# Performance work log

Hardware: AMD Instinct MI355X
Metric: run time of the kernel (lower is better)

Reference implementation:

```python
import jax, jax.numpy as jnp
import numpy as np
from jax import lax

T, B, R = 128, 128, 512  # timesteps, batch_size, read_size


def setup_inputs() -> dict:
    key = jax.random.key(0)
    ks = jax.random.split(key, 5)
    return {
        "u":  jax.random.uniform(ks[0], (T, B, 1), dtype=jnp.float32),
        "d1": jax.random.uniform(ks[1], (T, B, 1), dtype=jnp.float32),
        "d2": jax.random.uniform(ks[2], (T, B, 1), dtype=jnp.float32),
        "v1": jax.random.normal(ks[3], (T, B, R), dtype=jnp.float32),
        "v2": jax.random.normal(ks[4], (T, B, R), dtype=jnp.float32),
    }


def _forward(u, d1, d2, v1, v2):
    # Stack-style neural memory: each step pushes two (strength, value) slots,
    # reads up to total strength u from the top of the stack, then pops strength u.
    Tn, Bn, _ = u.shape
    Rn = v1.shape[-1]
    nslots = 2 * Tn
    # Pre-allocated slot store; unused slots have S=0, V=0 and contribute exactly 0
    # to both the read summary and strength_used, matching the growing-list semantics.
    S0 = jnp.zeros((nslots, Bn, 1), dtype=u.dtype)
    V0 = jnp.zeros((nslots, Bn, Rn), dtype=v1.dtype)

    def step(carry, inp):
        S, V = carry
        u_t, d1_t, d2_t, v1_t, v2_t, t = inp
        # push(d1, d2, v1, v2)
        S = S.at[2 * t].set(d1_t).at[2 * t + 1].set(d2_t)
        V = V.at[2 * t].set(v1_t).at[2 * t + 1].set(v2_t)
        Srev = S[::-1]  # stack order: top (most recent) first
        Vrev = V[::-1]

        # read(u): sequential scan over slots with strength bookkeeping
        def read_step(c, sv):
            summary, used = c
            s_i, v_i = sv
            # NOTE: torch.max(u - strength_used) is a GLOBAL max over the (B,1)
            # tensor (0-dim scalar), faithfully reproduced here.
            scal = jnp.max(u_t - used)
            summary = summary + v_i * jnp.minimum(s_i, scal)
            return (summary, used + s_i), None

        (summary, _), _ = lax.scan(
            read_step,
            (jnp.zeros((Bn, Rn), u.dtype), jnp.zeros((Bn, 1), u.dtype)),
            (Srev, Vrev),
        )

        # pop(u): elementwise strength depletion, same slot order
        def pop_step(used, s_i):
            s_new = s_i - jnp.minimum(s_i, jnp.maximum(jnp.zeros_like(s_i), u_t - used))
            return used + s_i, s_new

        _, Srev_new = lax.scan(pop_step, jnp.zeros((Bn, 1), u.dtype), Srev)
        return (Srev_new[::-1], V), summary

    xs = (u, d1, d2, v1, v2, jnp.arange(Tn))
    (_, _), outs = lax.scan(step, (S0, V0), xs)
    return outs  # (T, B, R) read contents per step


def reference(u, d1, d2, v1, v2):
    return _forward(u, d1, d2, v1, v2)
```

## Files before the change

### kernel.cpp

```cpp
#include <hip/hip_runtime.h>
#include <hip/hip_bf16.h>
#include <math.h>

constexpr int T = 128;
constexpr int B = 128;
constexpr int R = 512;
constexpr int NS = 256;

typedef __attribute__((ext_vector_type(8))) short bf16x8;
typedef __attribute__((ext_vector_type(4))) float f32x4;

static __device__ __forceinline__ ushort f2bf(float f) {
    union { float f; unsigned u; } v; v.f = f;
    unsigned r = v.u + 0x7fffu + ((v.u >> 16) & 1u);
    return (ushort)(r >> 16);
}

__global__ __launch_bounds__(128) void hscan(
    const float* __restrict__ u, const float* __restrict__ d1,
    const float* __restrict__ d2, float* __restrict__ H)
{
    const int b    = blockIdx.x * 2 + (threadIdx.x >> 6);
    const int lane = threadIdx.x & 63;

    int idx = lane * B + b;
    float P = d1[idx] + d2[idx] - u[idx];
    #pragma unroll
    for (int off = 1; off < 64; off <<= 1) {
        float o = __shfl_up(P, off);
        if (lane >= off) P += o;
    }
    float M = P;
    #pragma unroll
    for (int off = 1; off < 64; off <<= 1) {
        float o = __shfl_up(M, off);
        if (lane >= off) M = fminf(M, o);
    }
    H[idx] = P - fminf(0.f, M);
    const float carryP = __shfl(P, 63);
    const float carryM = fminf(0.f, __shfl(M, 63));

    idx = (64 + lane) * B + b;
    float p2 = d1[idx] + d2[idx] - u[idx];
    #pragma unroll
    for (int off = 1; off < 64; off <<= 1) {
        float o = __shfl_up(p2, off);
        if (lane >= off) p2 += o;
    }
    float m2 = p2;
    #pragma unroll
    for (int off = 1; off < 64; off <<= 1) {
        float o = __shfl_up(m2, off);
        if (lane >= off) m2 = fminf(m2, o);
    }
    const float Pt = carryP + p2;
    H[idx] = Pt - fminf(carryM, carryP + m2);
}

__global__ __launch_bounds__(512) void weights(
    const float* __restrict__ u, const float* __restrict__ d1,
    const float* __restrict__ d2, const float* __restrict__ H,
    ushort* __restrict__ w)
{
    const int t    = blockIdx.x;
    const int tid  = threadIdx.x;
    const int wv   = tid >> 6;
    const int lane = tid & 63;
    __shared__ float smin[8][B];

    const int b0 = lane, b1 = lane + 64;

    {
        const int rs = wv * 16;
        const int re = min(rs + 16, t);
        float sa = 1e30f, sb = 1e30f;
        #pragma unroll 4
        for (int tau = rs; tau < re; ++tau) {
            sa = fminf(sa, H[tau * B + b0]);
            sb = fminf(sb, H[tau * B + b1]);
        }
        smin[wv][b0] = sa;
        smin[wv][b1] = sb;
    }
    __syncthreads();

    const float Ht1a = (t > 0) ? H[(t-1)*B + b0] : 0.f;
    const float Ht1b = (t > 0) ? H[(t-1)*B + b1] : 0.f;
    const float Hpa  = Ht1a + d1[t*B+b0] + d2[t*B+b0];
    const float Hpb  = Ht1b + d1[t*B+b1] + d2[t*B+b1];
    const float Aa   = u[t*B+b0] - Hpa;
    const float Ab   = u[t*B+b1] - Hpb;

    ushort* wrow0 = w + ((size_t)t * B + b0) * NS;
    ushort* wrow1 = w + ((size_t)t * B + b1) * NS;

    const int plo = wv * 16;
    if (plo <= t) {
        const int pe = min(plo + 15, t);
        float ma = 1e30f, mb = 1e30f;
        #pragma unroll
        for (int s = 0; s < 8; ++s) {
            if (s > wv) { ma = fminf(ma, smin[s][b0]); mb = fminf(mb, smin[s][b1]); }
        }
        float vala = (pe < t) ? H[pe*B + b0] : 0.f;
        float valb = (pe < t) ? H[pe*B + b1] : 0.f;
        float basea = (pe > 0) ? H[(pe-1)*B + b0] : 0.f;
        float baseb = (pe > 0) ? H[(pe-1)*B + b1] : 0.f;
        float pnb_a = (pe > 1) ? H[(pe-2)*B + b0] : 0.f;
        float pnb_b = (pe > 1) ? H[(pe-2)*B + b1] : 0.f;
        float nd1a = d1[pe*B+b0], nd1b = d1[pe*B+b1];
        float nd2a = d2[pe*B+b0], nd2b = d2[pe*B+b1];
        float s2a = 0.f, s3a = 0.f, s2b = 0.f, s3b = 0.f;

        for (int p = pe; p >= plo; --p) {
            const float d1a = nd1a, d1b = nd1b, d2a = nd2a, d2b = nd2b;
            if (p > plo) {
                nd1a = d1[(p-1)*B+b0]; nd1b = d1[(p-1)*B+b1];
                nd2a = d2[(p-1)*B+b0]; nd2b = d2[(p-1)*B+b1];
            }
            if (p < t) { ma = fminf(ma, vala); mb = fminf(mb, valb); }
            const float top0a = basea + d1a, top0b = baseb + d1b;
            const float top1a = top0a + d2a, top1b = top0b + d2b;

            const float sa0 = fminf(fmaxf(ma - basea, 0.f), d1a);
            const float sb0 = fminf(fmaxf(mb - baseb, 0.f), d1b);
            const float sa1 = fminf(fmaxf(ma - top0a, 0.f), d2a);
            const float sb1 = fminf(fmaxf(mb - top0b, 0.f), d2b);

            float cand0 = fmaxf(Aa + fminf(top0a, ma), Ab + fminf(top0b, mb));
            float cand1 = fmaxf(Aa + fminf(top1a, ma), Ab + fminf(top1b, mb));
            #pragma unroll
            for (int off = 32; off >= 1; off >>= 1) {
                cand0 = fmaxf(cand0, __shfl_xor(cand0, off));
                cand1 = fmaxf(cand1, __shfl_xor(cand1, off));
            }

            const float w0a = fminf(sa0, cand0), w0b = fminf(sb0, cand0);
            const float w1a = fminf(sa1, cand1), w1b = fminf(sb1, cand1);
            if (p & 1) { s2a = w0a; s3a = w1a; s2b = w0b; s3b = w1b; }
            else {
                const int g = p >> 1;
                *(ushort4*)(wrow0 + 4*g) =
                    make_ushort4(f2bf(w0a), f2bf(w1a), f2bf(s2a), f2bf(s3a));
                *(ushort4*)(wrow1 + 4*g) =
                    make_ushort4(f2bf(w0b), f2bf(w1b), f2bf(s2b), f2bf(s3b));
            }
            vala = basea; valb = baseb;
            basea = pnb_a; baseb = pnb_b;
            if (p - 2 >= plo) {
                pnb_a = (p >= 3) ? H[(p-3)*B + b0] : 0.f;
                pnb_b = (p >= 3) ? H[(p-3)*B + b1] : 0.f;
            }
        }
    }

    const int gstart = (t >> 1) + 1;
    const int ng = (NS / 4) - gstart;
    if (ng > 0) {
        const ushort4 z = make_ushort4(0, 0, 0, 0);
        const int total = ng * B;
        for (int idx = tid; idx < total; idx += 512) {
            const int gi = idx % ng;
            const int bb = idx / ng;
            *(ushort4*)(w + ((size_t)t*B + bb)*NS + 4*(gstart + gi)) = z;
        }
    }
}

#define RT 128
__global__ __launch_bounds__(512) void gemm_mfma(
    const ushort* __restrict__ w, const float* __restrict__ v1,
    const float* __restrict__ v2, float* __restrict__ out)
{
    const int b    = blockIdx.x;
    const int r0   = blockIdx.y * RT;
    const int tid  = threadIdx.x;
    const int wv   = tid >> 6;
    const int lane = tid & 63;

    __shared__ ushort As[2][128][40];
    __shared__ ushort Bs[2][128][40];

    const int arow = tid >> 2;
    const int ajh  = (tid & 3) * 8;
    const ushort* abase = w + ((size_t)arow * B + b) * NS + ajh;

    const int p2   = tid & 15;
    const int rseg = tid >> 4;
    const float* v1b = v1 + (size_t)b * R + r0 + rseg * 4;
    const float* v2b = v2 + (size_t)b * R + r0 + rseg * 4;

    f32x4 acc[8];
    const f32x4 zz = {0.f, 0.f, 0.f, 0.f};
    #pragma unroll
    for (int i = 0; i < 8; ++i) acc[i] = zz;

    uint4 la;
    float4 lv1, lv2;

    #define STAGE_LOAD(c) do {                                          \
        if (arow >= 16 * (c)) {                                         \
            la = *(const uint4*)(abase + (c) * 32);                     \
        } else {                                                        \
            la = make_uint4(0u, 0u, 0u, 0u);                            \
        }                                                               \
        const size_t off_ = (size_t)((c) * 16 + p2) * B * R;            \
        lv1 = *(const float4*)(v1b + off_);                             \
        lv2 = *(const float4*)(v2b + off_);                             \
    } while (0)

    #define STAGE_WRITE(buf) do {                                       \
        *(uint4*)&As[buf][arow][ajh] = la;                              \
        const float* f1_ = (const float*)&lv1;                          \
        const float* f2_ = (const float*)&lv2;                          \
        _Pragma("unroll")                                               \
        for (int i_ = 0; i_ < 4; ++i_) {                                \
            unsigned pk_ = (unsigned)f2bf(f1_[i_]) |                    \
                           ((unsigned)f2bf(f2_[i_]) << 16);             \
            *(unsigned*)&Bs[buf][rseg * 4 + i_][p2 * 2] = pk_;          \
        }                                                               \
    } while (0)

    const int tb = wv * 16 + (lane & 15);
    const int ko = (lane >> 4) * 8;

    STAGE_LOAD(0);
    STAGE_WRITE(0);
    #pragma unroll
    for (int c = 0; c < 8; ++c) {
        const int buf = c & 1;
        if (c < 7) STAGE_LOAD(c + 1);
        __syncthreads();
        if (c <= wv) {
            bf16x8 a0 = *(const bf16x8*)&As[buf][tb][ko];
            #pragma unroll
            for (int cf = 0; cf < 8; ++cf) {
                bf16x8 bb = *(const bf16x8*)&Bs[buf][cf*16 + (lane & 15)][ko];
                acc[cf] = __builtin_amdgcn_mfma_f32_16x16x32_bf16(a0, bb, acc[cf], 0, 0, 0);
            }
        }
        if (c < 7) STAGE_WRITE((c + 1) & 1);
    }

    const int dcol  = lane & 15;
    const int drow4 = (lane >> 4) * 4;
    #pragma unroll
    for (int cf = 0; cf < 8; ++cf) {
        const int rg = r0 + cf * 16 + dcol;
        #pragma unroll
        for (int i = 0; i < 4; ++i) {
            const int tg = wv * 16 + drow4 + i;
            out[((size_t)tg * B + b) * R + rg] = acc[cf][i];
        }
    }
    #undef STAGE_LOAD
    #undef STAGE_WRITE
}

extern "C" void kernel_launch(void* const* d_in, const int* in_sizes, int n_in,
                              void* d_out, int out_size, void* d_ws, size_t ws_size,
                              hipStream_t stream) {
    const float* u  = (const float*)d_in[0];
    const float* d1 = (const float*)d_in[1];
    const float* d2 = (const float*)d_in[2];
    const float* v1 = (const float*)d_in[3];
    const float* v2 = (const float*)d_in[4];
    float* out = (float*)d_out;

    const size_t welems = (size_t)T * B * NS;
    ushort* w = (ushort*)d_ws;
    float* H;
    if (ws_size >= welems * sizeof(ushort) + (size_t)T * B * sizeof(float)) {
        H = (float*)((char*)d_ws + welems * sizeof(ushort));
    } else {
        H = (float*)d_out;
    }

    hscan  <<<dim3(B / 2), dim3(128), 0, stream>>>(u, d1, d2, H);
    weights<<<dim3(T),     dim3(512), 0, stream>>>(u, d1, d2, H, w);
    gemm_mfma<<<dim3(B, R / RT), dim3(512), 0, stream>>>(w, v1, v2, out);
}
```

Before: 43.26 us.

## Stage H in LDS for weights and deepen GEMM prefetch to three buffers

The weights kernel now copies the first t rows of H into a shared-memory array before the scan. All later H reads, including the per-iteration base and value loads, come from LDS, which replaces the register-rotation prefetch scheme over global memory. The GEMM kernel moves from double to triple LDS buffering and keeps two register stages of global loads in flight, so each chunk is loaded two iterations ahead while keeping one barrier per iteration. In exchange, the weights kernel uses up to 64KB of extra LDS, which may lower occupancy, and the GEMM kernel needs more registers and LDS.

```diff
diff --git a/kernel.cpp b/kernel.cpp
--- a/kernel.cpp
+++ b/kernel.cpp
@@ -66,7 +66,14 @@
     const int tid  = threadIdx.x;
     const int wv   = tid >> 6;
     const int lane = tid & 63;
+    __shared__ float eH[T][B];
     __shared__ float smin[8][B];
+
+    const int nfl = t * B;
+    for (int i = tid * 4; i < nfl; i += 2048) {
+        *(float4*)(&eH[0][0] + i) = *(const float4*)(H + i);
+    }
+    __syncthreads();
 
     const int b0 = lane, b1 = lane + 64;
 
@@ -74,18 +81,17 @@
         const int rs = wv * 16;
         const int re = min(rs + 16, t);
         float sa = 1e30f, sb = 1e30f;
-        #pragma unroll 4
         for (int tau = rs; tau < re; ++tau) {
-            sa = fminf(sa, H[tau * B + b0]);
-            sb = fminf(sb, H[tau * B + b1]);
+            sa = fminf(sa, eH[tau][b0]);
+            sb = fminf(sb, eH[tau][b1]);
         }
         smin[wv][b0] = sa;
         smin[wv][b1] = sb;
     }
     __syncthreads();
 
-    const float Ht1a = (t > 0) ? H[(t-1)*B + b0] : 0.f;
-    const float Ht1b = (t > 0) ? H[(t-1)*B + b1] : 0.f;
+    const float Ht1a = (t > 0) ? eH[t-1][b0] : 0.f;
+    const float Ht1b = (t > 0) ? eH[t-1][b1] : 0.f;
     const float Hpa  = Ht1a + d1[t*B+b0] + d2[t*B+b0];
     const float Hpb  = Ht1b + d1[t*B+b1] + d2[t*B+b1];
     const float Aa   = u[t*B+b0] - Hpa;
@@ -102,23 +108,18 @@
         for (int s = 0; s < 8; ++s) {
             if (s > wv) { ma = fminf(ma, smin[s][b0]); mb = fminf(mb, smin[s][b1]); }
         }
-        float vala = (pe < t) ? H[pe*B + b0] : 0.f;
-        float valb = (pe < t) ? H[pe*B + b1] : 0.f;
-        float basea = (pe > 0) ? H[(pe-1)*B + b0] : 0.f;
-        float baseb = (pe > 0) ? H[(pe-1)*B + b1] : 0.f;
-        float pnb_a = (pe > 1) ? H[(pe-2)*B + b0] : 0.f;
-        float pnb_b = (pe > 1) ? H[(pe-2)*B + b1] : 0.f;
+        float s2a = 0.f, s3a = 0.f, s2b = 0.f, s3b = 0.f;
         float nd1a = d1[pe*B+b0], nd1b = d1[pe*B+b1];
         float nd2a = d2[pe*B+b0], nd2b = d2[pe*B+b1];
-        float s2a = 0.f, s3a = 0.f, s2b = 0.f, s3b = 0.f;
-
         for (int p = pe; p >= plo; --p) {
             const float d1a = nd1a, d1b = nd1b, d2a = nd2a, d2b = nd2b;
             if (p > plo) {
                 nd1a = d1[(p-1)*B+b0]; nd1b = d1[(p-1)*B+b1];
                 nd2a = d2[(p-1)*B+b0]; nd2b = d2[(p-1)*B+b1];
             }
-            if (p < t) { ma = fminf(ma, vala); mb = fminf(mb, valb); }
+            if (p < t) { ma = fminf(ma, eH[p][b0]); mb = fminf(mb, eH[p][b1]); }
+            const float basea = (p > 0) ? eH[p-1][b0] : 0.f;
+            const float baseb = (p > 0) ? eH[p-1][b1] : 0.f;
             const float top0a = basea + d1a, top0b = baseb + d1b;
             const float top1a = top0a + d2a, top1b = top0b + d2b;
 
@@ -144,12 +145,6 @@
                     make_ushort4(f2bf(w0a), f2bf(w1a), f2bf(s2a), f2bf(s3a));
                 *(ushort4*)(wrow1 + 4*g) =
                     make_ushort4(f2bf(w0b), f2bf(w1b), f2bf(s2b), f2bf(s3b));
-            }
-            vala = basea; valb = baseb;
-            basea = pnb_a; baseb = pnb_b;
-            if (p - 2 >= plo) {
-                pnb_a = (p >= 3) ? H[(p-3)*B + b0] : 0.f;
-                pnb_b = (p >= 3) ? H[(p-3)*B + b1] : 0.f;
             }
         }
     }
@@ -178,8 +173,8 @@
     const int wv   = tid >> 6;
     const int lane = tid & 63;
 
-    __shared__ ushort As[2][128][40];
-    __shared__ ushort Bs[2][128][40];
+    __shared__ ushort As[3][128][40];
+    __shared__ ushort Bs[3][128][40];
 
     const int arow = tid >> 2;
     const int ajh  = (tid & 3) * 8;
@@ -195,24 +190,26 @@
     #pragma unroll
     for (int i = 0; i < 8; ++i) acc[i] = zz;
 
-    uint4 la;
-    float4 lv1, lv2;
-
-    #define STAGE_LOAD(c) do {                                          \
-        if (arow >= 16 * (c)) {                                         \
-            la = *(const uint4*)(abase + (c) * 32);                     \
-        } else {                                                        \
-            la = make_uint4(0u, 0u, 0u, 0u);                            \
+    uint4 la[2];
+    float4 lv1[2], lv2[2];
+
+    #define STAGE_LOAD(s, c) do {                                       \
+        if ((c) < 8) {                                                  \
+            if (arow >= 16 * (c)) {                                     \
+                la[s] = *(const uint4*)(abase + (c) * 32);              \
+            } else {                                                    \
+                la[s] = make_uint4(0u, 0u, 0u, 0u);                     \
+            }                                                           \
+            const size_t off_ = (size_t)((c) * 16 + p2) * B * R;        \
+            lv1[s] = *(const float4*)(v1b + off_);                      \
+            lv2[s] = *(const float4*)(v2b + off_);                      \
         }                                                               \
-        const size_t off_ = (size_t)((c) * 16 + p2) * B * R;            \
-        lv1 = *(const float4*)(v1b + off_);                             \
-        lv2 = *(const float4*)(v2b + off_);                             \
     } while (0)
 
-    #define STAGE_WRITE(buf) do {                                       \
-        *(uint4*)&As[buf][arow][ajh] = la;                              \
-        const float* f1_ = (const float*)&lv1;                          \
-        const float* f2_ = (const float*)&lv2;                          \
+    #define STAGE_WRITE(s, buf) do {                                    \
+        *(uint4*)&As[buf][arow][ajh] = la[s];                           \
+        const float* f1_ = (const float*)&lv1[s];                       \
+        const float* f2_ = (const float*)&lv2[s];                       \
         _Pragma("unroll")                                               \
         for (int i_ = 0; i_ < 4; ++i_) {                                \
             unsigned pk_ = (unsigned)f2bf(f1_[i_]) |                    \
@@ -224,22 +221,23 @@
     const int tb = wv * 16 + (lane & 15);
     const int ko = (lane >> 4) * 8;
 
-    STAGE_LOAD(0);
-    STAGE_WRITE(0);
+    STAGE_LOAD(0, 0);
+    STAGE_WRITE(0, 0);
+    STAGE_LOAD(1, 1);
+
     #pragma unroll
     for (int c = 0; c < 8; ++c) {
-        const int buf = c & 1;
-        if (c < 7) STAGE_LOAD(c + 1);
+        STAGE_LOAD(c & 1, c + 2);
         __syncthreads();
         if (c <= wv) {
-            bf16x8 a0 = *(const bf16x8*)&As[buf][tb][ko];
+            bf16x8 a0 = *(const bf16x8*)&As[c % 3][tb][ko];
             #pragma unroll
             for (int cf = 0; cf < 8; ++cf) {
-                bf16x8 bb = *(const bf16x8*)&Bs[buf][cf*16 + (lane & 15)][ko];
+                bf16x8 bb = *(const bf16x8*)&Bs[c % 3][cf*16 + (lane & 15)][ko];
                 acc[cf] = __builtin_amdgcn_mfma_f32_16x16x32_bf16(a0, bb, acc[cf], 0, 0, 0);
             }
         }
-        if (c < 7) STAGE_WRITE((c + 1) & 1);
+        if (c < 7) STAGE_WRITE((c + 1) & 1, (c + 1) % 3);
     }
 
     const int dcol  = lane & 15;
```

Result: faster. 42.40 us (-2.0%).
